# Optimization experiments

Hardware: AMD Instinct MI355X
Metric: run time of the kernel (lower is better)

Reference implementation:

```python
import jax, jax.numpy as jnp
import numpy as np

N_NODES = 50000
N_EDGES = 800000
N_GRAPHS = 512
D = 128


def _gcn_layer(x, W, b, src, dst, norm):
    # PyG GCNConv: h = x @ W; out[i] = sum_{j->i} norm_ji * h[j]; out += b
    h = x @ W                                   # [N, D]
    msg = h[src] * norm[:, None]                # [E+N, D] gathered messages
    out = jax.ops.segment_sum(msg, dst, num_segments=N_NODES)
    return out + b


def setup_inputs() -> dict:
    key = jax.random.key(0)
    ks = jax.random.split(key, 9)
    inp = {
        "x": jax.random.normal(ks[0], (N_NODES, D), dtype=jnp.float32),
        "W1": jax.random.normal(ks[1], (D, D), dtype=jnp.float32) * 0.05,
        "b1": jax.random.normal(ks[2], (D,), dtype=jnp.float32) * 0.05,
        "W2": jax.random.normal(ks[3], (D, D), dtype=jnp.float32) * 0.05,
        "b2": jax.random.normal(ks[4], (D,), dtype=jnp.float32) * 0.05,
        "W3": jax.random.normal(ks[5], (D, D), dtype=jnp.float32) * 0.05,
        "b3": jax.random.normal(ks[6], (D,), dtype=jnp.float32) * 0.05,
        "edge_index": jax.random.randint(ks[7], (2, N_EDGES), 0, N_NODES, dtype=jnp.int64),
        "batch_vec": jnp.sort(jax.random.randint(ks[8], (N_NODES,), 0, N_GRAPHS, dtype=jnp.int64)),
    }
    return inp


def reference(x, W1, b1, W2, b2, W3, b3, edge_index, batch_vec):
    # Add self-loops (GCNConv default) and compute symmetric normalization.
    loops = jnp.arange(N_NODES, dtype=edge_index.dtype)
    src = jnp.concatenate([edge_index[0], loops])   # [E+N]
    dst = jnp.concatenate([edge_index[1], loops])   # [E+N]
    deg = jax.ops.segment_sum(jnp.ones_like(dst, dtype=x.dtype), dst,
                              num_segments=N_NODES)
    dis = jnp.where(deg > 0, jax.lax.rsqrt(jnp.maximum(deg, 1.0)), 0.0)
    norm = dis[src] * dis[dst]                      # [E+N]

    h = jax.nn.relu(_gcn_layer(x, W1, b1, src, dst, norm))
    h = jax.nn.relu(_gcn_layer(h, W2, b2, src, dst, norm))
    h = jax.nn.relu(_gcn_layer(h, W3, b3, src, dst, norm))

    # global_add_pool: per-graph sum over nodes.
    return jax.ops.segment_sum(h, batch_vec, num_segments=N_GRAPHS)  # [G, D]
```

## Files before the change

### kernel.cpp

```cpp
#include <hip/hip_runtime.h>

#define N_NODES 50000
#define N_EDGES 800000
#define N_GRAPHS 512
#define DIM 128
#define N_PAD 50048

#define BW_LOG 9
#define BWID 512
#define NB ((N_NODES + BWID - 1) / BWID)
#define CHUNK 4096
#define NCHUNK ((N_EDGES + CHUNK - 1) / CHUNK)

typedef unsigned int uint;
typedef unsigned short ushort;
typedef __attribute__((ext_vector_type(8))) short bf16x8;
typedef __attribute__((ext_vector_type(4))) float f32x4;

__device__ __forceinline__ ushort f2bf(float f) {
    uint u = __float_as_uint(f);
    return (ushort)((u + 0x7fffu + ((u >> 16) & 1u)) >> 16);
}
__device__ __forceinline__ float bf2f(ushort h) { return __uint_as_float((uint)h << 16); }
__device__ __forceinline__ float bflo(uint p) { return __uint_as_float(p << 16); }
__device__ __forceinline__ float bfhi(uint p) { return __uint_as_float(p & 0xffff0000u); }


__global__ __launch_bounds__(256) void bhist_k(const int* __restrict__ dst,
                                               int* __restrict__ bcnt_pad, int e) {
    __shared__ int h[NB];
    int t = threadIdx.x;
    for (int i = t; i < NB; i += 256) h[i] = 0;
    __syncthreads();
    int base = blockIdx.x * CHUNK;
    for (int i = t; i < CHUNK; i += 256) {
        int idx = base + i;
        if (idx < e) atomicAdd(&h[dst[idx] >> BW_LOG], 1);
    }
    __syncthreads();
    for (int i = t; i < NB; i += 256)
        if (h[i]) atomicAdd(&bcnt_pad[i << 4], h[i]);
}

__global__ void bscan_k(const int* __restrict__ bcnt_pad, int* __restrict__ bbase,
                        int* __restrict__ bcur_pad) {
    __shared__ int v[128];
    int t = threadIdx.x;
    int x = (t < NB) ? bcnt_pad[t << 4] : 0;
    v[t] = x;
    __syncthreads();
    for (int o = 1; o < 128; o <<= 1) {
        int val = v[t];
        int add = (t >= o) ? v[t - o] : 0;
        __syncthreads();
        v[t] = val + add;
        __syncthreads();
    }
    if (t < NB) {
        int excl = (t == 0) ? 0 : v[t - 1];
        bbase[t] = excl;
        bcur_pad[t << 4] = excl;
    }
    if (t == NB - 1) bbase[NB] = v[t];
}

__global__ __launch_bounds__(256) void bscat_k(const int* __restrict__ src,
                                               const int* __restrict__ dst,
                                               int* __restrict__ bcur_pad,
                                               uint* __restrict__ stage, int e) {
    __shared__ int h[NB];
    __shared__ int bb[NB];
    __shared__ int lc[NB];
    int t = threadIdx.x;
    for (int i = t; i < NB; i += 256) h[i] = 0;
    __syncthreads();
    int base = blockIdx.x * CHUNK;
    for (int i = t; i < CHUNK; i += 256) {
        int idx = base + i;
        if (idx < e) atomicAdd(&h[dst[idx] >> BW_LOG], 1);
    }
    __syncthreads();
    for (int i = t; i < NB; i += 256) {
        int c = h[i];
        bb[i] = c ? atomicAdd(&bcur_pad[i << 4], c) : 0;
        lc[i] = 0;
    }
    __syncthreads();
    for (int i = t; i < CHUNK; i += 256) {
        int idx = base + i;
        if (idx < e) {
            int d = dst[idx];
            int b = d >> BW_LOG;
            int r = atomicAdd(&lc[b], 1);
            stage[bb[b] + r] = ((uint)src[idx] << BW_LOG) | (uint)(d & (BWID - 1));
        }
    }
}

__global__ __launch_bounds__(256) void csr_k(const uint* __restrict__ stage,
                                             const int* __restrict__ bbase,
                                             int* __restrict__ row_ptr,
                                             float* __restrict__ dis,
                                             int* __restrict__ col) {
    __shared__ int hist[BWID];
    __shared__ int excl[BWID];
    __shared__ int ws[256];
    int b = blockIdx.x, t = threadIdx.x;
    int beg = bbase[b], end = bbase[b + 1];
    for (int i = t; i < BWID; i += 256) hist[i] = 0;
    __syncthreads();
    for (int i = beg + t; i < end; i += 256)
        atomicAdd(&hist[stage[i] & (BWID - 1)], 1);
    __syncthreads();
    int s = hist[2 * t] + hist[2 * t + 1];
    ws[t] = s;
    __syncthreads();
    for (int o = 1; o < 256; o <<= 1) {
        int v = ws[t];
        int add = (t >= o) ? ws[t - o] : 0;
        __syncthreads();
        ws[t] = v + add;
        __syncthreads();
    }
    int pre = (t == 0) ? 0 : ws[t - 1];
    excl[2 * t] = pre;
    excl[2 * t + 1] = pre + hist[2 * t];
    __syncthreads();
    int node0 = b * BWID;
    for (int i = t; i < BWID; i += 256) {
        int node = node0 + i;
        if (node < N_NODES) {
            row_ptr[node] = beg + excl[i];
            dis[node] = rsqrtf((float)(hist[i] + 1));
        } else if (node == N_NODES) {
            row_ptr[node] = beg + excl[i];
        }
    }
    __syncthreads();
    for (int i = t; i < BWID; i += 256) hist[i] = excl[i];
    __syncthreads();
    for (int i = beg + t; i < end; i += 256) {
        uint p = stage[i];
        int d9 = p & (BWID - 1);
        int r = atomicAdd(&hist[d9], 1);
        col[beg + r] = (int)(p >> BW_LOG);
    }
}


__global__ void wconv_k(const float* __restrict__ Wa, const float* __restrict__ Wb,
                        const float* __restrict__ Wc, ushort* __restrict__ Whi,
                        ushort* __restrict__ Wlo) {
    int i = blockIdx.x * 256 + threadIdx.x;
    int layer = i >> 14, r = i & 16383;
    const float* W = layer == 0 ? Wa : (layer == 1 ? Wb : Wc);
    int k = r >> 7, nn = r & 127;
    float w = W[r];
    ushort h = f2bf(w);
    size_t o = (size_t)layer * DIM * DIM + nn * 128 + k;
    Whi[o] = h;
    Wlo[o] = f2bf(w - bf2f(h));
}


template <typename TIn>
__global__ __launch_bounds__(256) void gemm_mfma_k(const TIn* __restrict__ X,
                                                   const ushort* __restrict__ Whi,
                                                   const ushort* __restrict__ Wlo,
                                                   ushort* __restrict__ H, int n) {
    __shared__ __align__(16) ushort lds[128 * 136];
    int t = threadIdx.x;

    auto stageW = [&](const ushort* Wsw) {
#pragma unroll
        for (int j = 0; j < 8; j++) {
            int idx8 = t + j * 256;
            int nn = idx8 >> 4;
            int k0 = (idx8 & 15) * 8;
            uint4 v = ((const uint4*)Wsw)[idx8];
            *(uint4*)&lds[nn * 136 + k0] = v;
        }
    };

    stageW(Whi);

    int w = t >> 6, l = t & 63;
    int quad = l >> 4, lr = l & 15;
    int arow = blockIdx.x * 64 + w * 16 + lr;
    int srow = arow < n ? arow : n - 1;

    bf16x8 a[4], alo[4];
#pragma unroll
    for (int q = 0; q < 4; q++) {
        if constexpr (sizeof(TIn) == 4) {
            const float4* xp = (const float4*)(X + (size_t)srow * DIM + q * 32 + quad * 8);
            float4 v0 = xp[0], v1 = xp[1];
            float f[8] = {v0.x, v0.y, v0.z, v0.w, v1.x, v1.y, v1.z, v1.w};
            bf16x8 ah, al;
#pragma unroll
            for (int j = 0; j < 8; j++) {
                ushort h = f2bf(f[j]);
                ah[j] = (short)h;
                al[j] = (short)f2bf(f[j] - bf2f(h));
            }
            a[q] = ah;
            alo[q] = al;
        } else {
            a[q] = *(const bf16x8*)(X + (size_t)srow * DIM + q * 32 + quad * 8);
        }
    }

    f32x4 acc[8];
#pragma unroll
    for (int c = 0; c < 8; c++) acc[c] = (f32x4){0.f, 0.f, 0.f, 0.f};

    __syncthreads();
#pragma unroll
    for (int q = 0; q < 4; q++) {
#pragma unroll
        for (int c = 0; c < 8; c++) {
            bf16x8 b = *(const bf16x8*)&lds[(c * 16 + lr) * 136 + q * 32 + quad * 8];
            acc[c] = __builtin_amdgcn_mfma_f32_16x16x32_bf16(a[q], b, acc[c], 0, 0, 0);
            if constexpr (sizeof(TIn) == 4)
                acc[c] = __builtin_amdgcn_mfma_f32_16x16x32_bf16(alo[q], b, acc[c], 0, 0, 0);
        }
    }

    __syncthreads();
    stageW(Wlo);
    __syncthreads();
#pragma unroll
    for (int q = 0; q < 4; q++) {
#pragma unroll
        for (int c = 0; c < 8; c++) {
            bf16x8 b = *(const bf16x8*)&lds[(c * 16 + lr) * 136 + q * 32 + quad * 8];
            acc[c] = __builtin_amdgcn_mfma_f32_16x16x32_bf16(a[q], b, acc[c], 0, 0, 0);
        }
    }

    __syncthreads();
#pragma unroll
    for (int c = 0; c < 8; c++) {
#pragma unroll
        for (int r = 0; r < 4; r++) {
            int rl = w * 16 + quad * 4 + r;
            lds[rl * 136 + c * 16 + lr] = f2bf(acc[c][r]);
        }
    }
    __syncthreads();
#pragma unroll
    for (int j = 0; j < 4; j++) {
        int idx = t + j * 256;
        int rl = idx >> 4, sl = idx & 15;
        int grow = blockIdx.x * 64 + rl;
        if (grow < n) {
            uint4 v = *(const uint4*)&lds[rl * 136 + sl * 8];
            ((uint4*)(H + (size_t)grow * DIM))[sl] = v;
        }
    }
}


#define AGG_BODY                                                                 \
    const ushort* Hl = H + lane * 8;                                             \
    float dn = dis[node];                                                        \
    int beg = row_ptr[node], end = row_ptr[node + 1];                            \
    uint4 pw = *(const uint4*)(Hl + (size_t)node * DIM);                         \
    a0 = dn * bflo(pw.x); a1 = dn * bfhi(pw.x);                                  \
    a2 = dn * bflo(pw.y); a3 = dn * bfhi(pw.y);                                  \
    a4 = dn * bflo(pw.z); a5 = dn * bfhi(pw.z);                                  \
    a6 = dn * bflo(pw.w); a7 = dn * bfhi(pw.w);                                  \
    int e = beg;                                                                 \
    for (; e + 3 < end; e += 4) {                                                \
        int c0 = col[e], c1 = col[e + 1], c2 = col[e + 2], c3 = col[e + 3];      \
        float w0 = dis[c0], w1 = dis[c1], w2 = dis[c2], w3 = dis[c3];            \
        uint4 p0 = *(const uint4*)(Hl + (size_t)c0 * DIM);                       \
        uint4 p1 = *(const uint4*)(Hl + (size_t)c1 * DIM);                       \
        uint4 p2 = *(const uint4*)(Hl + (size_t)c2 * DIM);                       \
        uint4 p3 = *(const uint4*)(Hl + (size_t)c3 * DIM);                       \
        a0 += w0 * bflo(p0.x) + w1 * bflo(p1.x) + w2 * bflo(p2.x) + w3 * bflo(p3.x); \
        a1 += w0 * bfhi(p0.x) + w1 * bfhi(p1.x) + w2 * bfhi(p2.x) + w3 * bfhi(p3.x); \
        a2 += w0 * bflo(p0.y) + w1 * bflo(p1.y) + w2 * bflo(p2.y) + w3 * bflo(p3.y); \
        a3 += w0 * bfhi(p0.y) + w1 * bfhi(p1.y) + w2 * bfhi(p2.y) + w3 * bfhi(p3.y); \
        a4 += w0 * bflo(p0.z) + w1 * bflo(p1.z) + w2 * bflo(p2.z) + w3 * bflo(p3.z); \
        a5 += w0 * bfhi(p0.z) + w1 * bfhi(p1.z) + w2 * bfhi(p2.z) + w3 * bfhi(p3.z); \
        a6 += w0 * bflo(p0.w) + w1 * bflo(p1.w) + w2 * bflo(p2.w) + w3 * bflo(p3.w); \
        a7 += w0 * bfhi(p0.w) + w1 * bfhi(p1.w) + w2 * bfhi(p2.w) + w3 * bfhi(p3.w); \
    }                                                                            \
    for (; e < end; e++) {                                                       \
        int c = col[e];                                                          \
        float w = dis[c];                                                        \
        uint4 p = *(const uint4*)(Hl + (size_t)c * DIM);                         \
        a0 += w * bflo(p.x); a1 += w * bfhi(p.x);                                \
        a2 += w * bflo(p.y); a3 += w * bfhi(p.y);                                \
        a4 += w * bflo(p.z); a5 += w * bfhi(p.z);                                \
        a6 += w * bflo(p.w); a7 += w * bfhi(p.w);                                \
    }                                                                            \
    a0 = fmaxf(a0 * dn + bias[d0], 0.f);                                         \
    a1 = fmaxf(a1 * dn + bias[d0 + 1], 0.f);                                     \
    a2 = fmaxf(a2 * dn + bias[d0 + 2], 0.f);                                     \
    a3 = fmaxf(a3 * dn + bias[d0 + 3], 0.f);                                     \
    a4 = fmaxf(a4 * dn + bias[d0 + 4], 0.f);                                     \
    a5 = fmaxf(a5 * dn + bias[d0 + 5], 0.f);                                     \
    a6 = fmaxf(a6 * dn + bias[d0 + 6], 0.f);                                     \
    a7 = fmaxf(a7 * dn + bias[d0 + 7], 0.f);

__global__ __launch_bounds__(256) void agg_k(const ushort* __restrict__ H,
                                             const int* __restrict__ row_ptr,
                                             const int* __restrict__ col,
                                             const float* __restrict__ dis,
                                             const float* __restrict__ bias,
                                             ushort* __restrict__ Out, int n) {
    int node = blockIdx.x * 16 + (threadIdx.x >> 4);
    int lane = threadIdx.x & 15;
    if (node >= n) return;
    int d0 = lane * 8;
    float a0, a1, a2, a3, a4, a5, a6, a7;
    AGG_BODY
    uint4 o;
    o.x = (uint)f2bf(a0) | ((uint)f2bf(a1) << 16);
    o.y = (uint)f2bf(a2) | ((uint)f2bf(a3) << 16);
    o.z = (uint)f2bf(a4) | ((uint)f2bf(a5) << 16);
    o.w = (uint)f2bf(a6) | ((uint)f2bf(a7) << 16);
    *(uint4*)(Out + (size_t)node * DIM + d0) = o;
}

__global__ __launch_bounds__(256) void agg_pool_k(const ushort* __restrict__ H,
                                                  const int* __restrict__ row_ptr,
                                                  const int* __restrict__ col,
                                                  const float* __restrict__ dis,
                                                  const float* __restrict__ bias,
                                                  const int* __restrict__ batch,
                                                  float* __restrict__ Out, int n) {
    __shared__ float acc[DIM];
    int t = threadIdx.x;
    int node = blockIdx.x * 16 + (t >> 4);
    int lane = t & 15;
    int d0 = lane * 8;
    float a0 = 0.f, a1 = 0.f, a2 = 0.f, a3 = 0.f, a4 = 0.f, a5 = 0.f, a6 = 0.f, a7 = 0.f;
    int g = -1;
    if (node < n) {
        AGG_BODY
        g = batch[node];
    }
    int first = blockIdx.x * 16;
    int last = first + 15 < n ? first + 15 : n - 1;
    int g0 = batch[first], g1 = batch[last];
    for (int gr = g0; gr <= g1; gr++) {
        if (t < DIM) acc[t] = 0.f;
        __syncthreads();
        if (g == gr) {
            atomicAdd(&acc[d0], a0);
            atomicAdd(&acc[d0 + 1], a1);
            atomicAdd(&acc[d0 + 2], a2);
            atomicAdd(&acc[d0 + 3], a3);
            atomicAdd(&acc[d0 + 4], a4);
            atomicAdd(&acc[d0 + 5], a5);
            atomicAdd(&acc[d0 + 6], a6);
            atomicAdd(&acc[d0 + 7], a7);
        }
        __syncthreads();
        if (t < DIM) atomicAdd(&Out[gr * DIM + t], acc[t]);
        __syncthreads();
    }
}


extern "C" void kernel_launch(void* const* d_in, const int* in_sizes, int n_in,
                              void* d_out, int out_size, void* d_ws, size_t ws_size,
                              hipStream_t stream) {
    const float* x  = (const float*)d_in[0];
    const float* W1 = (const float*)d_in[1];
    const float* b1 = (const float*)d_in[2];
    const float* W2 = (const float*)d_in[3];
    const float* b2 = (const float*)d_in[4];
    const float* W3 = (const float*)d_in[5];
    const float* b3 = (const float*)d_in[6];
    const int*   ei = (const int*)d_in[7];
    const int*   bv = (const int*)d_in[8];
    float* out = (float*)d_out;

    const int N = N_NODES, E = N_EDGES;

    char* p = (char*)d_ws;
    auto alloc = [&](size_t bytes) -> void* {
        void* r = (void*)p;
        p += (bytes + 255) & ~(size_t)255;
        return r;
    };
    int*    bcnt_pad = (int*)alloc((size_t)NB * 16 * 4);
    int*    bcur_pad = (int*)alloc((size_t)NB * 16 * 4);
    int*    bbase    = (int*)alloc((size_t)(NB + 1) * 4);
    int*    row_ptr  = (int*)alloc((size_t)(N + 1) * 4);
    float*  dis      = (float*)alloc((size_t)N * 4);
    uint*   stage    = (uint*)alloc((size_t)E * 4);
    int*    col      = (int*)alloc((size_t)E * 4);
    ushort* B1       = (ushort*)alloc((size_t)N_PAD * DIM * 2);
    ushort* B2       = (ushort*)alloc((size_t)N_PAD * DIM * 2);

    ushort* Whi = (ushort*)stage;
    ushort* Wlo = Whi + (size_t)3 * DIM * DIM;

    const int* src = ei;
    const int* dst = ei + E;

    hipMemsetAsync(d_out, 0, (size_t)N_GRAPHS * DIM * sizeof(float), stream);
    hipMemsetAsync(bcnt_pad, 0, (size_t)NB * 16 * 4, stream);

    bhist_k<<<NCHUNK, 256, 0, stream>>>(dst, bcnt_pad, E);
    bscan_k<<<1, 128, 0, stream>>>(bcnt_pad, bbase, bcur_pad);
    bscat_k<<<NCHUNK, 256, 0, stream>>>(src, dst, bcur_pad, stage, E);
    csr_k<<<NB, 256, 0, stream>>>(stage, bbase, row_ptr, dis, col);

    wconv_k<<<192, 256, 0, stream>>>(W1, W2, W3, Whi, Wlo);

    int gemm_grid = N_PAD / 64;
    int agg_grid  = (N + 15) / 16;

    gemm_mfma_k<float><<<gemm_grid, 256, 0, stream>>>(x, Whi, Wlo, B1, N);
    agg_k<<<agg_grid, 256, 0, stream>>>(B1, row_ptr, col, dis, b1, B2, N);

    gemm_mfma_k<ushort><<<gemm_grid, 256, 0, stream>>>(B2, Whi + (size_t)DIM * DIM,
                                                       Wlo + (size_t)DIM * DIM, B1, N);
    agg_k<<<agg_grid, 256, 0, stream>>>(B1, row_ptr, col, dis, b2, B2, N);

    gemm_mfma_k<ushort><<<gemm_grid, 256, 0, stream>>>(B2, Whi + (size_t)2 * DIM * DIM,
                                                       Wlo + (size_t)2 * DIM * DIM, B1, N);
    agg_pool_k<<<agg_grid, 256, 0, stream>>>(B1, row_ptr, col, dis, b3, bv, out, N);
}
```

Baseline: 287.9 us.

## Fuse aggregation with next-layer GEMM and co-launch preprocessing with first GEMM

Merges the weight conversion into the histogram kernel and the first GEMM into the scatter kernel as extra blocks, so independent work shares a launch. Each aggregation is fused with the next layer's GEMM. The GEMM output is pre-scaled by the source-node dis, which removes the per-edge dis gather in later aggregations. Launch count and one full H round-trip per layer go away. In exchange, the fused kernel uses 4 threads per node with 32 fp32 accumulators each, a large LDS footprint (about 52KB), and more register pressure that can lower occupancy for the latency-bound gather.

```diff
diff --git a/kernel.cpp b/kernel.cpp
--- a/kernel.cpp
+++ b/kernel.cpp
@@ -26,20 +26,37 @@
 __device__ __forceinline__ float bfhi(uint p) { return __uint_as_float(p & 0xffff0000u); }
 
 
-__global__ __launch_bounds__(256) void bhist_k(const int* __restrict__ dst,
-                                               int* __restrict__ bcnt_pad, int e) {
-    __shared__ int h[NB];
+__global__ __launch_bounds__(256) void bhist_wconv_k(const int* __restrict__ dst,
+                                                     int* __restrict__ bcnt_pad, int e,
+                                                     const float* __restrict__ Wa,
+                                                     const float* __restrict__ Wb,
+                                                     const float* __restrict__ Wc,
+                                                     ushort* __restrict__ Whi,
+                                                     ushort* __restrict__ Wlo) {
     int t = threadIdx.x;
-    for (int i = t; i < NB; i += 256) h[i] = 0;
-    __syncthreads();
-    int base = blockIdx.x * CHUNK;
-    for (int i = t; i < CHUNK; i += 256) {
-        int idx = base + i;
-        if (idx < e) atomicAdd(&h[dst[idx] >> BW_LOG], 1);
-    }
-    __syncthreads();
-    for (int i = t; i < NB; i += 256)
-        if (h[i]) atomicAdd(&bcnt_pad[i << 4], h[i]);
+    if (blockIdx.x < NCHUNK) {
+        __shared__ int h[NB];
+        for (int i = t; i < NB; i += 256) h[i] = 0;
+        __syncthreads();
+        int base = blockIdx.x * CHUNK;
+        for (int i = t; i < CHUNK; i += 256) {
+            int idx = base + i;
+            if (idx < e) atomicAdd(&h[dst[idx] >> BW_LOG], 1);
+        }
+        __syncthreads();
+        for (int i = t; i < NB; i += 256)
+            if (h[i]) atomicAdd(&bcnt_pad[i << 4], h[i]);
+        return;
+    }
+    int i = (blockIdx.x - NCHUNK) * 256 + t;
+    int layer = i >> 14, r = i & 16383;
+    const float* W = layer == 0 ? Wa : (layer == 1 ? Wb : Wc);
+    int k = r >> 7, nn = r & 127;
+    float w = W[r];
+    ushort h = f2bf(w);
+    size_t o = (size_t)layer * DIM * DIM + nn * 128 + k;
+    Whi[o] = h;
+    Wlo[o] = f2bf(w - bf2f(h));
 }
 
 __global__ void bscan_k(const int* __restrict__ bcnt_pad, int* __restrict__ bbase,
@@ -64,35 +81,127 @@
     if (t == NB - 1) bbase[NB] = v[t];
 }
 
-__global__ __launch_bounds__(256) void bscat_k(const int* __restrict__ src,
-                                               const int* __restrict__ dst,
-                                               int* __restrict__ bcur_pad,
-                                               uint* __restrict__ stage, int e) {
-    __shared__ int h[NB];
-    __shared__ int bb[NB];
-    __shared__ int lc[NB];
+
+__global__ __launch_bounds__(256) void bscat_gemm1_k(const int* __restrict__ src,
+                                                     const int* __restrict__ dst,
+                                                     int* __restrict__ bcur_pad,
+                                                     uint* __restrict__ stage, int e,
+                                                     const float* __restrict__ X,
+                                                     const ushort* __restrict__ Whi,
+                                                     const ushort* __restrict__ Wlo,
+                                                     ushort* __restrict__ H, int n) {
+    __shared__ __align__(16) ushort smem[128 * 136];
     int t = threadIdx.x;
-    for (int i = t; i < NB; i += 256) h[i] = 0;
-    __syncthreads();
-    int base = blockIdx.x * CHUNK;
-    for (int i = t; i < CHUNK; i += 256) {
-        int idx = base + i;
-        if (idx < e) atomicAdd(&h[dst[idx] >> BW_LOG], 1);
-    }
-    __syncthreads();
-    for (int i = t; i < NB; i += 256) {
-        int c = h[i];
-        bb[i] = c ? atomicAdd(&bcur_pad[i << 4], c) : 0;
-        lc[i] = 0;
-    }
-    __syncthreads();
-    for (int i = t; i < CHUNK; i += 256) {
-        int idx = base + i;
-        if (idx < e) {
-            int d = dst[idx];
-            int b = d >> BW_LOG;
-            int r = atomicAdd(&lc[b], 1);
-            stage[bb[b] + r] = ((uint)src[idx] << BW_LOG) | (uint)(d & (BWID - 1));
+
+    if (blockIdx.x < NCHUNK) {
+        int* h  = (int*)smem;
+        int* bb = h + NB;
+        int* lc = bb + NB;
+        for (int i = t; i < NB; i += 256) h[i] = 0;
+        __syncthreads();
+        int base = blockIdx.x * CHUNK;
+        for (int i = t; i < CHUNK; i += 256) {
+            int idx = base + i;
+            if (idx < e) atomicAdd(&h[dst[idx] >> BW_LOG], 1);
+        }
+        __syncthreads();
+        for (int i = t; i < NB; i += 256) {
+            int c = h[i];
+            bb[i] = c ? atomicAdd(&bcur_pad[i << 4], c) : 0;
+            lc[i] = 0;
+        }
+        __syncthreads();
+        for (int i = t; i < CHUNK; i += 256) {
+            int idx = base + i;
+            if (idx < e) {
+                int d = dst[idx];
+                int b = d >> BW_LOG;
+                int r = atomicAdd(&lc[b], 1);
+                stage[bb[b] + r] = ((uint)src[idx] << BW_LOG) | (uint)(d & (BWID - 1));
+            }
+        }
+        return;
+    }
+
+    ushort* lds = smem;
+    int gb = blockIdx.x - NCHUNK;
+    auto stageW = [&](const ushort* Wsw) {
+#pragma unroll
+        for (int j = 0; j < 8; j++) {
+            int idx8 = t + j * 256;
+            int nn = idx8 >> 4;
+            int k0 = (idx8 & 15) * 8;
+            uint4 v = ((const uint4*)Wsw)[idx8];
+            *(uint4*)&lds[nn * 136 + k0] = v;
+        }
+    };
+    stageW(Whi);
+
+    int w = t >> 6, l = t & 63;
+    int quad = l >> 4, lr = l & 15;
+    int arow = gb * 64 + w * 16 + lr;
+    int srow = arow < n ? arow : n - 1;
+
+    bf16x8 a[4], alo[4];
+#pragma unroll
+    for (int q = 0; q < 4; q++) {
+        const float4* xp = (const float4*)(X + (size_t)srow * DIM + q * 32 + quad * 8);
+        float4 v0 = xp[0], v1 = xp[1];
+        float f[8] = {v0.x, v0.y, v0.z, v0.w, v1.x, v1.y, v1.z, v1.w};
+        bf16x8 ah, al;
+#pragma unroll
+        for (int j = 0; j < 8; j++) {
+            ushort hh = f2bf(f[j]);
+            ah[j] = (short)hh;
+            al[j] = (short)f2bf(f[j] - bf2f(hh));
+        }
+        a[q] = ah;
+        alo[q] = al;
+    }
+
+    f32x4 acc[8];
+#pragma unroll
+    for (int c = 0; c < 8; c++) acc[c] = (f32x4){0.f, 0.f, 0.f, 0.f};
+
+    __syncthreads();
+#pragma unroll
+    for (int q = 0; q < 4; q++) {
+#pragma unroll
+        for (int c = 0; c < 8; c++) {
+            bf16x8 b = *(const bf16x8*)&lds[(c * 16 + lr) * 136 + q * 32 + quad * 8];
+            acc[c] = __builtin_amdgcn_mfma_f32_16x16x32_bf16(a[q], b, acc[c], 0, 0, 0);
+            acc[c] = __builtin_amdgcn_mfma_f32_16x16x32_bf16(alo[q], b, acc[c], 0, 0, 0);
+        }
+    }
+    __syncthreads();
+    stageW(Wlo);
+    __syncthreads();
+#pragma unroll
+    for (int q = 0; q < 4; q++) {
+#pragma unroll
+        for (int c = 0; c < 8; c++) {
+            bf16x8 b = *(const bf16x8*)&lds[(c * 16 + lr) * 136 + q * 32 + quad * 8];
+            acc[c] = __builtin_amdgcn_mfma_f32_16x16x32_bf16(a[q], b, acc[c], 0, 0, 0);
+        }
+    }
+    __syncthreads();
+#pragma unroll
+    for (int c = 0; c < 8; c++) {
+#pragma unroll
+        for (int r = 0; r < 4; r++) {
+            int rl = w * 16 + quad * 4 + r;
+            lds[rl * 136 + c * 16 + lr] = f2bf(acc[c][r]);
+        }
+    }
+    __syncthreads();
+#pragma unroll
+    for (int j = 0; j < 4; j++) {
+        int idx = t + j * 256;
+        int rl = idx >> 4, sl = idx & 15;
+        int grow = gb * 64 + rl;
+        if (grow < n) {
+            uint4 v = *(const uint4*)&lds[rl * 136 + sl * 8];
+            ((uint4*)(H + (size_t)grow * DIM))[sl] = v;
         }
     }
 }
@@ -148,28 +257,83 @@
 }
 
 
-__global__ void wconv_k(const float* __restrict__ Wa, const float* __restrict__ Wb,
-                        const float* __restrict__ Wc, ushort* __restrict__ Whi,
-                        ushort* __restrict__ Wlo) {
-    int i = blockIdx.x * 256 + threadIdx.x;
-    int layer = i >> 14, r = i & 16383;
-    const float* W = layer == 0 ? Wa : (layer == 1 ? Wb : Wc);
-    int k = r >> 7, nn = r & 127;
-    float w = W[r];
-    ushort h = f2bf(w);
-    size_t o = (size_t)layer * DIM * DIM + nn * 128 + k;
-    Whi[o] = h;
-    Wlo[o] = f2bf(w - bf2f(h));
-}
-
-
-template <typename TIn>
-__global__ __launch_bounds__(256) void gemm_mfma_k(const TIn* __restrict__ X,
-                                                   const ushort* __restrict__ Whi,
-                                                   const ushort* __restrict__ Wlo,
-                                                   ushort* __restrict__ H, int n) {
-    __shared__ __align__(16) ushort lds[128 * 136];
+template <bool EDGE_DIS>
+__global__ __launch_bounds__(256) void fused_agg_gemm_k(
+    const ushort* __restrict__ Hin, const int* __restrict__ row_ptr,
+    const int* __restrict__ col, const float* __restrict__ dis,
+    const float* __restrict__ bias, const ushort* __restrict__ Whi,
+    const ushort* __restrict__ Wlo, ushort* __restrict__ Hout, int n) {
+    __shared__ __align__(16) ushort wlds[128 * 136];
+    __shared__ __align__(16) ushort alds[64 * 136];
     int t = threadIdx.x;
+
+    int nl = t >> 2;
+    int lane = t & 3;
+    int node = blockIdx.x * 64 + nl;
+    int cnode = node < n ? node : n - 1;
+    float dn = dis[cnode];
+    int beg = row_ptr[cnode], end = row_ptr[cnode + 1];
+
+    float acc[32];
+    {
+        float ws = EDGE_DIS ? dn : 1.f;
+        const ushort* rp = Hin + (size_t)cnode * DIM + lane * 32;
+#pragma unroll
+        for (int k = 0; k < 4; k++) {
+            uint4 pv = *(const uint4*)(rp + k * 8);
+            acc[k * 8 + 0] = ws * bflo(pv.x); acc[k * 8 + 1] = ws * bfhi(pv.x);
+            acc[k * 8 + 2] = ws * bflo(pv.y); acc[k * 8 + 3] = ws * bfhi(pv.y);
+            acc[k * 8 + 4] = ws * bflo(pv.z); acc[k * 8 + 5] = ws * bfhi(pv.z);
+            acc[k * 8 + 6] = ws * bflo(pv.w); acc[k * 8 + 7] = ws * bfhi(pv.w);
+        }
+    }
+    for (int e = beg; e < end; e += 4) {
+        int ii[4];
+        float wv[4];
+#pragma unroll
+        for (int j = 0; j < 4; j++) {
+            int idx = e + j;
+            wv[j] = (idx < end) ? 1.f : 0.f;
+            ii[j] = idx < end ? idx : end - 1;
+        }
+        int c4[4];
+#pragma unroll
+        for (int j = 0; j < 4; j++) c4[j] = col[ii[j]];
+        if (EDGE_DIS) {
+#pragma unroll
+            for (int j = 0; j < 4; j++) wv[j] *= dis[c4[j]];
+        }
+#pragma unroll
+        for (int j = 0; j < 4; j++) {
+            const ushort* rp = Hin + (size_t)c4[j] * DIM + lane * 32;
+            float wj = wv[j];
+#pragma unroll
+            for (int k = 0; k < 4; k++) {
+                uint4 pv = *(const uint4*)(rp + k * 8);
+                acc[k * 8 + 0] += wj * bflo(pv.x); acc[k * 8 + 1] += wj * bfhi(pv.x);
+                acc[k * 8 + 2] += wj * bflo(pv.y); acc[k * 8 + 3] += wj * bfhi(pv.y);
+                acc[k * 8 + 4] += wj * bflo(pv.z); acc[k * 8 + 5] += wj * bfhi(pv.z);
+                acc[k * 8 + 6] += wj * bflo(pv.w); acc[k * 8 + 7] += wj * bfhi(pv.w);
+            }
+        }
+    }
+#pragma unroll
+    for (int k = 0; k < 4; k++) {
+        float y0 = fmaxf(acc[k * 8 + 0] * dn + bias[lane * 32 + k * 8 + 0], 0.f);
+        float y1 = fmaxf(acc[k * 8 + 1] * dn + bias[lane * 32 + k * 8 + 1], 0.f);
+        float y2 = fmaxf(acc[k * 8 + 2] * dn + bias[lane * 32 + k * 8 + 2], 0.f);
+        float y3 = fmaxf(acc[k * 8 + 3] * dn + bias[lane * 32 + k * 8 + 3], 0.f);
+        float y4 = fmaxf(acc[k * 8 + 4] * dn + bias[lane * 32 + k * 8 + 4], 0.f);
+        float y5 = fmaxf(acc[k * 8 + 5] * dn + bias[lane * 32 + k * 8 + 5], 0.f);
+        float y6 = fmaxf(acc[k * 8 + 6] * dn + bias[lane * 32 + k * 8 + 6], 0.f);
+        float y7 = fmaxf(acc[k * 8 + 7] * dn + bias[lane * 32 + k * 8 + 7], 0.f);
+        uint4 o;
+        o.x = (uint)f2bf(y0) | ((uint)f2bf(y1) << 16);
+        o.y = (uint)f2bf(y2) | ((uint)f2bf(y3) << 16);
+        o.z = (uint)f2bf(y4) | ((uint)f2bf(y5) << 16);
+        o.w = (uint)f2bf(y6) | ((uint)f2bf(y7) << 16);
+        *(uint4*)&alds[nl * 136 + lane * 32 + k * 8] = o;
+    }
 
     auto stageW = [&](const ushort* Wsw) {
 #pragma unroll
@@ -178,73 +342,59 @@
             int nn = idx8 >> 4;
             int k0 = (idx8 & 15) * 8;
             uint4 v = ((const uint4*)Wsw)[idx8];
-            *(uint4*)&lds[nn * 136 + k0] = v;
+            *(uint4*)&wlds[nn * 136 + k0] = v;
         }
     };
-
     stageW(Whi);
+    __syncthreads();
 
     int w = t >> 6, l = t & 63;
     int quad = l >> 4, lr = l & 15;
-    int arow = blockIdx.x * 64 + w * 16 + lr;
-    int srow = arow < n ? arow : n - 1;
-
-    bf16x8 a[4], alo[4];
+    int arl = w * 16 + lr;
+    bf16x8 a[4];
+#pragma unroll
+    for (int q = 0; q < 4; q++)
+        a[q] = *(const bf16x8*)&alds[arl * 136 + q * 32 + quad * 8];
+
+    f32x4 gacc[8];
+#pragma unroll
+    for (int c = 0; c < 8; c++) gacc[c] = (f32x4){0.f, 0.f, 0.f, 0.f};
+
 #pragma unroll
     for (int q = 0; q < 4; q++) {
-        if constexpr (sizeof(TIn) == 4) {
-            const float4* xp = (const float4*)(X + (size_t)srow * DIM + q * 32 + quad * 8);
-            float4 v0 = xp[0], v1 = xp[1];
-            float f[8] = {v0.x, v0.y, v0.z, v0.w, v1.x, v1.y, v1.z, v1.w};
-            bf16x8 ah, al;
-#pragma unroll
-            for (int j = 0; j < 8; j++) {
-                ushort h = f2bf(f[j]);
-                ah[j] = (short)h;
-                al[j] = (short)f2bf(f[j] - bf2f(h));
-            }
-            a[q] = ah;
-            alo[q] = al;
-        } else {
-            a[q] = *(const bf16x8*)(X + (size_t)srow * DIM + q * 32 + quad * 8);
-        }
-    }
-
-    f32x4 acc[8];
-#pragma unroll
-    for (int c = 0; c < 8; c++) acc[c] = (f32x4){0.f, 0.f, 0.f, 0.f};
-
+#pragma unroll
+        for (int c = 0; c < 8; c++) {
+            bf16x8 b = *(const bf16x8*)&wlds[(c * 16 + lr) * 136 + q * 32 + quad * 8];
+            gacc[c] = __builtin_amdgcn_mfma_f32_16x16x32_bf16(a[q], b, gacc[c], 0, 0, 0);
+        }
+    }
+    __syncthreads();
+    stageW(Wlo);
     __syncthreads();
 #pragma unroll
     for (int q = 0; q < 4; q++) {
 #pragma unroll
         for (int c = 0; c < 8; c++) {
-            bf16x8 b = *(const bf16x8*)&lds[(c * 16 + lr) * 136 + q * 32 + quad * 8];
-            acc[c] = __builtin_amdgcn_mfma_f32_16x16x32_bf16(a[q], b, acc[c], 0, 0, 0);
-            if constexpr (sizeof(TIn) == 4)
-                acc[c] = __builtin_amdgcn_mfma_f32_16x16x32_bf16(alo[q], b, acc[c], 0, 0, 0);
-        }
-    }
-
-    __syncthreads();
-    stageW(Wlo);
-    __syncthreads();
-#pragma unroll
-    for (int q = 0; q < 4; q++) {
-#pragma unroll
-        for (int c = 0; c < 8; c++) {
-            bf16x8 b = *(const bf16x8*)&lds[(c * 16 + lr) * 136 + q * 32 + quad * 8];
-            acc[c] = __builtin_amdgcn_mfma_f32_16x16x32_bf16(a[q], b, acc[c], 0, 0, 0);
-        }
-    }
-
+            bf16x8 b = *(const bf16x8*)&wlds[(c * 16 + lr) * 136 + q * 32 + quad * 8];
+            gacc[c] = __builtin_amdgcn_mfma_f32_16x16x32_bf16(a[q], b, gacc[c], 0, 0, 0);
+        }
+    }
+
+    float dsc[4];
+    int orow0 = blockIdx.x * 64 + w * 16 + quad * 4;
+#pragma unroll
+    for (int r = 0; r < 4; r++) {
+        int rr = orow0 + r;
+        if (rr > n - 1) rr = n - 1;
+        dsc[r] = dis[rr];
+    }
     __syncthreads();
 #pragma unroll
     for (int c = 0; c < 8; c++) {
 #pragma unroll
         for (int r = 0; r < 4; r++) {
             int rl = w * 16 + quad * 4 + r;
-            lds[rl * 136 + c * 16 + lr] = f2bf(acc[c][r]);
+            alds[rl * 136 + c * 16 + lr] = f2bf(gacc[c][r] * dsc[r]);
         }
     }
     __syncthreads();
@@ -254,76 +404,12 @@
         int rl = idx >> 4, sl = idx & 15;
         int grow = blockIdx.x * 64 + rl;
         if (grow < n) {
-            uint4 v = *(const uint4*)&lds[rl * 136 + sl * 8];
-            ((uint4*)(H + (size_t)grow * DIM))[sl] = v;
-        }
-    }
-}
-
-
-#define AGG_BODY                                                                 \
-    const ushort* Hl = H + lane * 8;                                             \
-    float dn = dis[node];                                                        \
-    int beg = row_ptr[node], end = row_ptr[node + 1];                            \
-    uint4 pw = *(const uint4*)(Hl + (size_t)node * DIM);                         \
-    a0 = dn * bflo(pw.x); a1 = dn * bfhi(pw.x);                                  \
-    a2 = dn * bflo(pw.y); a3 = dn * bfhi(pw.y);                                  \
-    a4 = dn * bflo(pw.z); a5 = dn * bfhi(pw.z);                                  \
-    a6 = dn * bflo(pw.w); a7 = dn * bfhi(pw.w);                                  \
-    int e = beg;                                                                 \
-    for (; e + 3 < end; e += 4) {                                                \
-        int c0 = col[e], c1 = col[e + 1], c2 = col[e + 2], c3 = col[e + 3];      \
-        float w0 = dis[c0], w1 = dis[c1], w2 = dis[c2], w3 = dis[c3];            \
-        uint4 p0 = *(const uint4*)(Hl + (size_t)c0 * DIM);                       \
-        uint4 p1 = *(const uint4*)(Hl + (size_t)c1 * DIM);                       \
-        uint4 p2 = *(const uint4*)(Hl + (size_t)c2 * DIM);                       \
-        uint4 p3 = *(const uint4*)(Hl + (size_t)c3 * DIM);                       \
-        a0 += w0 * bflo(p0.x) + w1 * bflo(p1.x) + w2 * bflo(p2.x) + w3 * bflo(p3.x); \
-        a1 += w0 * bfhi(p0.x) + w1 * bfhi(p1.x) + w2 * bfhi(p2.x) + w3 * bfhi(p3.x); \
-        a2 += w0 * bflo(p0.y) + w1 * bflo(p1.y) + w2 * bflo(p2.y) + w3 * bflo(p3.y); \
-        a3 += w0 * bfhi(p0.y) + w1 * bfhi(p1.y) + w2 * bfhi(p2.y) + w3 * bfhi(p3.y); \
-        a4 += w0 * bflo(p0.z) + w1 * bflo(p1.z) + w2 * bflo(p2.z) + w3 * bflo(p3.z); \
-        a5 += w0 * bfhi(p0.z) + w1 * bfhi(p1.z) + w2 * bfhi(p2.z) + w3 * bfhi(p3.z); \
-        a6 += w0 * bflo(p0.w) + w1 * bflo(p1.w) + w2 * bflo(p2.w) + w3 * bflo(p3.w); \
-        a7 += w0 * bfhi(p0.w) + w1 * bfhi(p1.w) + w2 * bfhi(p2.w) + w3 * bfhi(p3.w); \
-    }                                                                            \
-    for (; e < end; e++) {                                                       \
-        int c = col[e];                                                          \
-        float w = dis[c];                                                        \
-        uint4 p = *(const uint4*)(Hl + (size_t)c * DIM);                         \
-        a0 += w * bflo(p.x); a1 += w * bfhi(p.x);                                \
-        a2 += w * bflo(p.y); a3 += w * bfhi(p.y);                                \
-        a4 += w * bflo(p.z); a5 += w * bfhi(p.z);                                \
-        a6 += w * bflo(p.w); a7 += w * bfhi(p.w);                                \
-    }                                                                            \
-    a0 = fmaxf(a0 * dn + bias[d0], 0.f);                                         \
-    a1 = fmaxf(a1 * dn + bias[d0 + 1], 0.f);                                     \
-    a2 = fmaxf(a2 * dn + bias[d0 + 2], 0.f);                                     \
-    a3 = fmaxf(a3 * dn + bias[d0 + 3], 0.f);                                     \
-    a4 = fmaxf(a4 * dn + bias[d0 + 4], 0.f);                                     \
-    a5 = fmaxf(a5 * dn + bias[d0 + 5], 0.f);                                     \
-    a6 = fmaxf(a6 * dn + bias[d0 + 6], 0.f);                                     \
-    a7 = fmaxf(a7 * dn + bias[d0 + 7], 0.f);
-
-__global__ __launch_bounds__(256) void agg_k(const ushort* __restrict__ H,
-                                             const int* __restrict__ row_ptr,
-                                             const int* __restrict__ col,
-                                             const float* __restrict__ dis,
-                                             const float* __restrict__ bias,
-                                             ushort* __restrict__ Out, int n) {
-    int node = blockIdx.x * 16 + (threadIdx.x >> 4);
-    int lane = threadIdx.x & 15;
-    if (node >= n) return;
-    int d0 = lane * 8;
-    float a0, a1, a2, a3, a4, a5, a6, a7;
-    AGG_BODY
-    uint4 o;
-    o.x = (uint)f2bf(a0) | ((uint)f2bf(a1) << 16);
-    o.y = (uint)f2bf(a2) | ((uint)f2bf(a3) << 16);
-    o.z = (uint)f2bf(a4) | ((uint)f2bf(a5) << 16);
-    o.w = (uint)f2bf(a6) | ((uint)f2bf(a7) << 16);
-    *(uint4*)(Out + (size_t)node * DIM + d0) = o;
-}
+            uint4 v = *(const uint4*)&alds[rl * 136 + sl * 8];
+            ((uint4*)(Hout + (size_t)grow * DIM))[sl] = v;
+        }
+    }
+}
+
 
 __global__ __launch_bounds__(256) void agg_pool_k(const ushort* __restrict__ H,
                                                   const int* __restrict__ row_ptr,
@@ -332,7 +418,7 @@
                                                   const float* __restrict__ bias,
                                                   const int* __restrict__ batch,
                                                   float* __restrict__ Out, int n) {
-    __shared__ float acc[DIM];
+    __shared__ float sacc[DIM];
     int t = threadIdx.x;
     int node = blockIdx.x * 16 + (t >> 4);
     int lane = t & 15;
@@ -340,27 +426,63 @@
     float a0 = 0.f, a1 = 0.f, a2 = 0.f, a3 = 0.f, a4 = 0.f, a5 = 0.f, a6 = 0.f, a7 = 0.f;
     int g = -1;
     if (node < n) {
-        AGG_BODY
+        const ushort* Hl = H + lane * 8;
+        float dn = dis[node];
+        int beg = row_ptr[node], end = row_ptr[node + 1];
+        uint4 pw = *(const uint4*)(Hl + (size_t)node * DIM);
+        a0 = bflo(pw.x); a1 = bfhi(pw.x);
+        a2 = bflo(pw.y); a3 = bfhi(pw.y);
+        a4 = bflo(pw.z); a5 = bfhi(pw.z);
+        a6 = bflo(pw.w); a7 = bfhi(pw.w);
+        for (int e = beg; e < end; e += 8) {
+            int c_[8];
+            float w_[8];
+            uint4 p_[8];
+#pragma unroll
+            for (int j = 0; j < 8; j++) {
+                int idx = e + j;
+                w_[j] = (idx < end) ? 1.f : 0.f;
+                idx = idx < end ? idx : end - 1;
+                c_[j] = col[idx];
+            }
+#pragma unroll
+            for (int j = 0; j < 8; j++) p_[j] = *(const uint4*)(Hl + (size_t)c_[j] * DIM);
+#pragma unroll
+            for (int j = 0; j < 8; j++) {
+                a0 += w_[j] * bflo(p_[j].x); a1 += w_[j] * bfhi(p_[j].x);
+                a2 += w_[j] * bflo(p_[j].y); a3 += w_[j] * bfhi(p_[j].y);
+                a4 += w_[j] * bflo(p_[j].z); a5 += w_[j] * bfhi(p_[j].z);
+                a6 += w_[j] * bflo(p_[j].w); a7 += w_[j] * bfhi(p_[j].w);
+            }
+        }
+        a0 = fmaxf(a0 * dn + bias[d0 + 0], 0.f);
+        a1 = fmaxf(a1 * dn + bias[d0 + 1], 0.f);
+        a2 = fmaxf(a2 * dn + bias[d0 + 2], 0.f);
+        a3 = fmaxf(a3 * dn + bias[d0 + 3], 0.f);
+        a4 = fmaxf(a4 * dn + bias[d0 + 4], 0.f);
+        a5 = fmaxf(a5 * dn + bias[d0 + 5], 0.f);
+        a6 = fmaxf(a6 * dn + bias[d0 + 6], 0.f);
+        a7 = fmaxf(a7 * dn + bias[d0 + 7], 0.f);
         g = batch[node];
     }
     int first = blockIdx.x * 16;
     int last = first + 15 < n ? first + 15 : n - 1;
     int g0 = batch[first], g1 = batch[last];
     for (int gr = g0; gr <= g1; gr++) {
-        if (t < DIM) acc[t] = 0.f;
+        if (t < DIM) sacc[t] = 0.f;
         __syncthreads();
         if (g == gr) {
-            atomicAdd(&acc[d0], a0);
-            atomicAdd(&acc[d0 + 1], a1);
-            atomicAdd(&acc[d0 + 2], a2);
-            atomicAdd(&acc[d0 + 3], a3);
-            atomicAdd(&acc[d0 + 4], a4);
-            atomicAdd(&acc[d0 + 5], a5);
-            atomicAdd(&acc[d0 + 6], a6);
-            atomicAdd(&acc[d0 + 7], a7);
-        }
-        __syncthreads();
-        if (t < DIM) atomicAdd(&Out[gr * DIM + t], acc[t]);
+            atomicAdd(&sacc[d0], a0);
+            atomicAdd(&sacc[d0 + 1], a1);
+            atomicAdd(&sacc[d0 + 2], a2);
+            atomicAdd(&sacc[d0 + 3], a3);
+            atomicAdd(&sacc[d0 + 4], a4);
+            atomicAdd(&sacc[d0 + 5], a5);
+            atomicAdd(&sacc[d0 + 6], a6);
+            atomicAdd(&sacc[d0 + 7], a7);
+        }
+        __syncthreads();
+        if (t < DIM) atomicAdd(&Out[gr * DIM + t], sacc[t]);
         __syncthreads();
     }
 }
@@ -397,9 +519,8 @@
     int*    col      = (int*)alloc((size_t)E * 4);
     ushort* B1       = (ushort*)alloc((size_t)N_PAD * DIM * 2);
     ushort* B2       = (ushort*)alloc((size_t)N_PAD * DIM * 2);
-
-    ushort* Whi = (ushort*)stage;
-    ushort* Wlo = Whi + (size_t)3 * DIM * DIM;
+    ushort* Whi      = (ushort*)alloc((size_t)3 * DIM * DIM * 2);
+    ushort* Wlo      = (ushort*)alloc((size_t)3 * DIM * DIM * 2);
 
     const int* src = ei;
     const int* dst = ei + E;
@@ -407,24 +528,18 @@
     hipMemsetAsync(d_out, 0, (size_t)N_GRAPHS * DIM * sizeof(float), stream);
     hipMemsetAsync(bcnt_pad, 0, (size_t)NB * 16 * 4, stream);
 
-    bhist_k<<<NCHUNK, 256, 0, stream>>>(dst, bcnt_pad, E);
+    bhist_wconv_k<<<NCHUNK + 192, 256, 0, stream>>>(dst, bcnt_pad, E, W1, W2, W3, Whi, Wlo);
     bscan_k<<<1, 128, 0, stream>>>(bcnt_pad, bbase, bcur_pad);
-    bscat_k<<<NCHUNK, 256, 0, stream>>>(src, dst, bcur_pad, stage, E);
+    bscat_gemm1_k<<<NCHUNK + N_PAD / 64, 256, 0, stream>>>(src, dst, bcur_pad, stage, E,
+                                                           x, Whi, Wlo, B1, N);
     csr_k<<<NB, 256, 0, stream>>>(stage, bbase, row_ptr, dis, col);
 
-    wconv_k<<<192, 256, 0, stream>>>(W1, W2, W3, Whi, Wlo);
-
-    int gemm_grid = N_PAD / 64;
-    int agg_grid  = (N + 15) / 16;
-
-    gemm_mfma_k<float><<<gemm_grid, 256, 0, stream>>>(x, Whi, Wlo, B1, N);
-    agg_k<<<agg_grid, 256, 0, stream>>>(B1, row_ptr, col, dis, b1, B2, N);
-
-    gemm_mfma_k<ushort><<<gemm_grid, 256, 0, stream>>>(B2, Whi + (size_t)DIM * DIM,
-                                                       Wlo + (size_t)DIM * DIM, B1, N);
-    agg_k<<<agg_grid, 256, 0, stream>>>(B1, row_ptr, col, dis, b2, B2, N);
-
-    gemm_mfma_k<ushort><<<gemm_grid, 256, 0, stream>>>(B2, Whi + (size_t)2 * DIM * DIM,
-                                                       Wlo + (size_t)2 * DIM * DIM, B1, N);
-    agg_pool_k<<<agg_grid, 256, 0, stream>>>(B1, row_ptr, col, dis, b3, bv, out, N);
-}
+    int gg = N_PAD / 64;
+    fused_agg_gemm_k<true><<<gg, 256, 0, stream>>>(B1, row_ptr, col, dis, b1,
+                                                   Whi + (size_t)DIM * DIM,
+                                                   Wlo + (size_t)DIM * DIM, B2, N);
+    fused_agg_gemm_k<false><<<gg, 256, 0, stream>>>(B2, row_ptr, col, dis, b2,
+                                                    Whi + (size_t)2 * DIM * DIM,
+                                                    Wlo + (size_t)2 * DIM * DIM, B1, N);
+    agg_pool_k<<<(N + 15) / 16, 256, 0, stream>>>(B1, row_ptr, col, dis, b3, bv, out, N);
+}
```

Measured after the change: 273.9 us. 4.8% less time.
